# Kernel optimization log

Measured on AMD Instinct MI355X. Metric: run time of the kernel, lower is better.

## Reference

```python
import jax, jax.numpy as jnp
import numpy as np

SCOPE = 5
MASK_MAG = 9999.0


def setup_inputs() -> dict:
    key = jax.random.key(0)
    k1, k2, k3, k4 = jax.random.split(key, 4)
    B, T, F = 32, 2048, 256
    dataInput = jax.random.normal(k1, (B, T, F), dtype=jnp.float32)
    seqInput = jax.random.randint(k2, (B,), 1, T + 1)  # valid lengths in [1, T]
    seqInput = seqInput.at[0].set(T)  # torch code requires max(seqInput) == T
    W = jax.random.normal(k3, (SCOPE, F), dtype=jnp.float32) * 0.05  # Linear(F*scope -> 1) weight, reshaped
    b = jax.random.normal(k4, (1,), dtype=jnp.float32) * 0.05
    return {"dataInput": dataInput, "seqInput": seqInput, "W": W, "b": b,
            "hiddenNoduleNumbers": F}


def reference(dataInput, seqInput, W, b, hiddenNoduleNumbers):
    # dataInput: [B, T, F]; W: [scope, F]; b: [1]; seqInput: [B] lengths.
    B, T, F = dataInput.shape
    scope = W.shape[0]
    # Zero-pad `scope` frames at the end (torch pads scope rows then slices v:T+v).
    padded = jnp.concatenate(
        [dataInput, jnp.zeros((B, scope, F), dtype=dataInput.dtype)], axis=1)
    # Sliding-window linear score computed on-the-fly (no [B,T,scope*F] concat):
    # score[b,t] = sum_v padded[b, t+v, :] . W[v] + b
    scores = b[0] + sum(
        jnp.einsum('btf,f->bt', padded[:, v:T + v, :], W[v])
        for v in range(scope))  # [B, T]
    # AttentionMask: +9999 for valid positions, -9999 past the length; combined via min.
    valid = jnp.arange(T)[None, :] < seqInput[:, None]
    mask = jnp.where(valid, MASK_MAG, -MASK_MAG).astype(scores.dtype)
    maskedScores = jnp.minimum(scores, mask)
    attentionWeight = jax.nn.softmax(maskedScores, axis=-1)[:, :, None]  # [B, T, 1]
    attentionResult = jnp.sum(dataInput * attentionWeight, axis=1)  # [B, F]
    return attentionResult, attentionWeight
```

## Files before the change

kernel.cpp:

```cpp
#include <hip/hip_runtime.h>
#include <cfloat>

#define SCOPE 5
#define MASK_MAG 9999.0f
constexpr int F = 256;
constexpr int TW = 32;
constexpr int WAVES = 4;

__global__ __launch_bounds__(256) void fused_kernel(
    const float* __restrict__ data, const float* __restrict__ W,
    const float* __restrict__ bias, const int* __restrict__ seq,
    float* __restrict__ scores, float* __restrict__ pacc,
    float* __restrict__ pm, float* __restrict__ ps, int T) {
    const int b = blockIdx.y;
    const int tid = threadIdx.x;
    const int lane = tid & 63;
    const int wid = tid >> 6;
    const int lane4 = lane * 4;
    const int widx = blockIdx.x * WAVES + wid;
    const int t0 = widx * TW;
    if (t0 >= T) return;
    const int npw = T / TW;
    const float* __restrict__ dBase = data + (size_t)b * T * F;
    float* __restrict__ sb = scores + (size_t)b * T;
    const float bv = bias[0];
    const int L = seq[b];

    float4 w[SCOPE];
    #pragma unroll
    for (int v = 0; v < SCOPE; ++v)
        w[v] = *(const float4*)(W + v * F + lane4);

    const float4 fz = make_float4(0.f, 0.f, 0.f, 0.f);
    float4 S[16];

#define LOADROW(slot, off) do { \
    if ((off) < TW + 4) { \
        const int uu = t0 + (off); \
        S[slot] = (uu < T) ? *(const float4*)(dBase + (size_t)uu * F + lane4) : fz; \
    } } while (0)
#define DOT4(a, b) ((a).x*(b).x + (a).y*(b).y + (a).z*(b).z + (a).w*(b).w)

    #pragma unroll
    for (int k = 0; k < 16; ++k) LOADROW(k, k);

    float m_run = -FLT_MAX, s_run = 0.f;
    float4 acc = fz;

    #pragma unroll
    for (int ii = 0; ii < 2; ++ii) {
        const int base = ii * 16;
        float sc[8];

        #pragma unroll
        for (int j = 0; j < 8; ++j) {
            float s = DOT4(S[j], w[0]) + DOT4(S[j+1], w[1]) + DOT4(S[j+2], w[2])
                    + DOT4(S[j+3], w[3]) + DOT4(S[j+4], w[4]);
            s += __shfl_xor(s, 32, 64);
            s += __shfl_xor(s, 16, 64);
            s += __shfl_xor(s,  8, 64);
            s += __shfl_xor(s,  4, 64);
            s += __shfl_xor(s,  2, 64);
            s += __shfl_xor(s,  1, 64);
            s += bv;
            const int t = t0 + base + j;
            if (lane == 0) sb[t] = s;
            sc[j] = fminf(s, (t < L) ? MASK_MAG : -MASK_MAG);
        }
        {
            float gm = fmaxf(fmaxf(fmaxf(sc[0], sc[1]), fmaxf(sc[2], sc[3])),
                             fmaxf(fmaxf(sc[4], sc[5]), fmaxf(sc[6], sc[7])));
            const float m_new = fmaxf(m_run, gm);
            const float corr = expf(m_run - m_new);
            float psum = 0.f; float4 ga = fz;
            #pragma unroll
            for (int j = 0; j < 8; ++j) {
                const float p = expf(sc[j] - m_new);
                psum += p;
                ga.x += p * S[j].x; ga.y += p * S[j].y;
                ga.z += p * S[j].z; ga.w += p * S[j].w;
            }
            s_run = s_run * corr + psum;
            acc.x = acc.x * corr + ga.x; acc.y = acc.y * corr + ga.y;
            acc.z = acc.z * corr + ga.z; acc.w = acc.w * corr + ga.w;
            m_run = m_new;
        }
        #pragma unroll
        for (int k = 0; k < 8; ++k) LOADROW(k, base + 16 + k);

        #pragma unroll
        for (int j = 8; j < 16; ++j) {
            float s = DOT4(S[j & 15], w[0]) + DOT4(S[(j+1) & 15], w[1])
                    + DOT4(S[(j+2) & 15], w[2]) + DOT4(S[(j+3) & 15], w[3])
                    + DOT4(S[(j+4) & 15], w[4]);
            s += __shfl_xor(s, 32, 64);
            s += __shfl_xor(s, 16, 64);
            s += __shfl_xor(s,  8, 64);
            s += __shfl_xor(s,  4, 64);
            s += __shfl_xor(s,  2, 64);
            s += __shfl_xor(s,  1, 64);
            s += bv;
            const int t = t0 + base + j;
            if (lane == 0) sb[t] = s;
            sc[j - 8] = fminf(s, (t < L) ? MASK_MAG : -MASK_MAG);
        }
        {
            float gm = fmaxf(fmaxf(fmaxf(sc[0], sc[1]), fmaxf(sc[2], sc[3])),
                             fmaxf(fmaxf(sc[4], sc[5]), fmaxf(sc[6], sc[7])));
            const float m_new = fmaxf(m_run, gm);
            const float corr = expf(m_run - m_new);
            float psum = 0.f; float4 ga = fz;
            #pragma unroll
            for (int j = 0; j < 8; ++j) {
                const float p = expf(sc[j] - m_new);
                psum += p;
                ga.x += p * S[8 + j].x; ga.y += p * S[8 + j].y;
                ga.z += p * S[8 + j].z; ga.w += p * S[8 + j].w;
            }
            s_run = s_run * corr + psum;
            acc.x = acc.x * corr + ga.x; acc.y = acc.y * corr + ga.y;
            acc.z = acc.z * corr + ga.z; acc.w = acc.w * corr + ga.w;
            m_run = m_new;
        }
        #pragma unroll
        for (int k = 0; k < 8; ++k) LOADROW(8 + k, base + 24 + k);
    }
#undef DOT4
#undef LOADROW

    const int pw = b * npw + widx;
    *reinterpret_cast<float4*>(pacc + (size_t)pw * F + lane4) = acc;
    if (lane == 0) { pm[pw] = m_run; ps[pw] = s_run; }
}

__global__ __launch_bounds__(256) void finalize_kernel(
    const float* __restrict__ scores, const float* __restrict__ pacc,
    const float* __restrict__ pm, const float* __restrict__ ps,
    const int* __restrict__ seq, float* __restrict__ out_res,
    float* __restrict__ out_w, int T, int npw) {
    const int b = blockIdx.x;
    const int tid = threadIdx.x;
    __shared__ float scale[64];
    __shared__ float MS[2];

    if (tid < 64) {
        const float m = pm[b * npw + tid];
        const float s = ps[b * npw + tid];
        float M = m;
        #pragma unroll
        for (int off = 32; off >= 1; off >>= 1) M = fmaxf(M, __shfl_xor(M, off, 64));
        const float e = expf(m - M);
        float se = e * s;
        #pragma unroll
        for (int off = 32; off >= 1; off >>= 1) se += __shfl_xor(se, off, 64);
        scale[tid] = e;
        if (tid == 0) { MS[0] = M; MS[1] = 1.0f / se; }
    }
    __syncthreads();
    const float M = MS[0], invS = MS[1];

    float o = 0.f;
    for (int i = 0; i < npw; ++i)
        o += scale[i] * pacc[((size_t)(b * npw + i)) * F + tid];
    out_res[(size_t)b * F + tid] = o * invS;

    const int L = seq[b];
    for (int t = tid; t < T; t += 256) {
        const float raw = scores[(size_t)b * T + t];
        const float msk = fminf(raw, (t < L) ? MASK_MAG : -MASK_MAG);
        out_w[(size_t)b * T + t] = expf(msk - M) * invS;
    }
}

extern "C" void kernel_launch(void* const* d_in, const int* in_sizes, int n_in,
                              void* d_out, int out_size, void* d_ws, size_t ws_size,
                              hipStream_t stream) {
    const float* data = (const float*)d_in[0];
    const int*   seq  = (const int*)d_in[1];
    const float* W    = (const float*)d_in[2];
    const float* bias = (const float*)d_in[3];

    const int B  = in_sizes[1];
    const int Fr = in_sizes[2] / SCOPE;
    const int T  = in_sizes[0] / (B * Fr);
    (void)Fr;
    const int npw = T / TW;

    float* out_res = (float*)d_out;
    float* out_w   = (float*)d_out + (size_t)B * F;

    float* scores = (float*)d_ws;
    float* pacc   = scores + (size_t)B * T;
    float* pm     = pacc + (size_t)B * npw * F;
    float* ps     = pm + (size_t)B * npw;

    dim3 g1(T / (WAVES * TW), B);
    fused_kernel<<<g1, 256, 0, stream>>>(data, W, bias, seq, scores, pacc, pm, ps, T);
    finalize_kernel<<<B, 256, 0, stream>>>(scores, pacc, pm, ps, seq, out_res, out_w, T, npw);
}
```

Before: 35.37 us.

## Halve per-wave tile, merge partials in-block, split finalize across parts

```diff
diff --git a/kernel.cpp b/kernel.cpp
--- a/kernel.cpp
+++ b/kernel.cpp
@@ -4,10 +4,25 @@
 #define SCOPE 5
 #define MASK_MAG 9999.0f
 constexpr int F = 256;
-constexpr int TW = 32;
+constexpr int TW = 16;
 constexpr int WAVES = 4;
 
-__global__ __launch_bounds__(256) void fused_kernel(
+template <int CTRL>
+__device__ __forceinline__ float dppadd(float x) {
+    int v = __builtin_amdgcn_update_dpp(0, __float_as_int(x), CTRL, 0xF, 0xF, true);
+    return x + __int_as_float(v);
+}
+__device__ __forceinline__ float wave_sum(float s) {
+    s = dppadd<0xB1>(s);
+    s = dppadd<0x4E>(s);
+    s = dppadd<0x141>(s);
+    s = dppadd<0x140>(s);
+    s += __shfl_xor(s, 16, 64);
+    s += __shfl_xor(s, 32, 64);
+    return s;
+}
+
+__global__ __launch_bounds__(256, 4) void fused_kernel(
     const float* __restrict__ data, const float* __restrict__ W,
     const float* __restrict__ bias, const int* __restrict__ seq,
     float* __restrict__ scores, float* __restrict__ pacc,
@@ -17,10 +32,7 @@
     const int lane = tid & 63;
     const int wid = tid >> 6;
     const int lane4 = lane * 4;
-    const int widx = blockIdx.x * WAVES + wid;
-    const int t0 = widx * TW;
-    if (t0 >= T) return;
-    const int npw = T / TW;
+    const int t0 = (blockIdx.x * WAVES + wid) * TW;
     const float* __restrict__ dBase = data + (size_t)b * T * F;
     float* __restrict__ sb = scores + (size_t)b * T;
     const float bv = bias[0];
@@ -35,10 +47,9 @@
     float4 S[16];
 
 #define LOADROW(slot, off) do { \
-    if ((off) < TW + 4) { \
-        const int uu = t0 + (off); \
-        S[slot] = (uu < T) ? *(const float4*)(dBase + (size_t)uu * F + lane4) : fz; \
-    } } while (0)
+    const int uu = t0 + (off); \
+    S[slot] = (uu < T) ? *(const float4*)(dBase + (size_t)uu * F + lane4) : fz; \
+    } while (0)
 #define DOT4(a, b) ((a).x*(b).x + (a).y*(b).y + (a).z*(b).z + (a).w*(b).w)
 
     #pragma unroll
@@ -46,110 +57,107 @@
 
     float m_run = -FLT_MAX, s_run = 0.f;
     float4 acc = fz;
-
-    #pragma unroll
-    for (int ii = 0; ii < 2; ++ii) {
-        const int base = ii * 16;
-        float sc[8];
-
+    float sc[8];
+
+    #pragma unroll
+    for (int j = 0; j < 8; ++j) {
+        float s = DOT4(S[j], w[0]) + DOT4(S[j+1], w[1]) + DOT4(S[j+2], w[2])
+                + DOT4(S[j+3], w[3]) + DOT4(S[j+4], w[4]);
+        s = wave_sum(s) + bv;
+        const int t = t0 + j;
+        if (lane == 0) sb[t] = s;
+        sc[j] = fminf(s, (t < L) ? MASK_MAG : -MASK_MAG);
+    }
+    {
+        float gm = fmaxf(fmaxf(fmaxf(sc[0], sc[1]), fmaxf(sc[2], sc[3])),
+                         fmaxf(fmaxf(sc[4], sc[5]), fmaxf(sc[6], sc[7])));
+        const float m_new = fmaxf(m_run, gm);
+        const float corr = expf(m_run - m_new);
+        float psum = 0.f; float4 ga = fz;
         #pragma unroll
         for (int j = 0; j < 8; ++j) {
-            float s = DOT4(S[j], w[0]) + DOT4(S[j+1], w[1]) + DOT4(S[j+2], w[2])
-                    + DOT4(S[j+3], w[3]) + DOT4(S[j+4], w[4]);
-            s += __shfl_xor(s, 32, 64);
-            s += __shfl_xor(s, 16, 64);
-            s += __shfl_xor(s,  8, 64);
-            s += __shfl_xor(s,  4, 64);
-            s += __shfl_xor(s,  2, 64);
-            s += __shfl_xor(s,  1, 64);
-            s += bv;
-            const int t = t0 + base + j;
-            if (lane == 0) sb[t] = s;
-            sc[j] = fminf(s, (t < L) ? MASK_MAG : -MASK_MAG);
+            const float p = expf(sc[j] - m_new);
+            psum += p;
+            ga.x += p * S[j].x; ga.y += p * S[j].y;
+            ga.z += p * S[j].z; ga.w += p * S[j].w;
         }
-        {
-            float gm = fmaxf(fmaxf(fmaxf(sc[0], sc[1]), fmaxf(sc[2], sc[3])),
-                             fmaxf(fmaxf(sc[4], sc[5]), fmaxf(sc[6], sc[7])));
-            const float m_new = fmaxf(m_run, gm);
-            const float corr = expf(m_run - m_new);
-            float psum = 0.f; float4 ga = fz;
-            #pragma unroll
-            for (int j = 0; j < 8; ++j) {
-                const float p = expf(sc[j] - m_new);
-                psum += p;
-                ga.x += p * S[j].x; ga.y += p * S[j].y;
-                ga.z += p * S[j].z; ga.w += p * S[j].w;
-            }
-            s_run = s_run * corr + psum;
-            acc.x = acc.x * corr + ga.x; acc.y = acc.y * corr + ga.y;
-            acc.z = acc.z * corr + ga.z; acc.w = acc.w * corr + ga.w;
-            m_run = m_new;
+        s_run = s_run * corr + psum;
+        acc.x = acc.x * corr + ga.x; acc.y = acc.y * corr + ga.y;
+        acc.z = acc.z * corr + ga.z; acc.w = acc.w * corr + ga.w;
+        m_run = m_new;
+    }
+    #pragma unroll
+    for (int k = 0; k < 4; ++k) LOADROW(k, 16 + k);
+
+    #pragma unroll
+    for (int j = 0; j < 8; ++j) {
+        float s = DOT4(S[(8+j) & 15], w[0]) + DOT4(S[(9+j) & 15], w[1])
+                + DOT4(S[(10+j) & 15], w[2]) + DOT4(S[(11+j) & 15], w[3])
+                + DOT4(S[(12+j) & 15], w[4]);
+        s = wave_sum(s) + bv;
+        const int t = t0 + 8 + j;
+        if (lane == 0) sb[t] = s;
+        sc[j] = fminf(s, (t < L) ? MASK_MAG : -MASK_MAG);
+    }
+    {
+        float gm = fmaxf(fmaxf(fmaxf(sc[0], sc[1]), fmaxf(sc[2], sc[3])),
+                         fmaxf(fmaxf(sc[4], sc[5]), fmaxf(sc[6], sc[7])));
+        const float m_new = fmaxf(m_run, gm);
+        const float corr = expf(m_run - m_new);
+        float psum = 0.f; float4 ga = fz;
+        #pragma unroll
+        for (int j = 0; j < 8; ++j) {
+            const float p = expf(sc[j] - m_new);
+            psum += p;
+            ga.x += p * S[8 + j].x; ga.y += p * S[8 + j].y;
+            ga.z += p * S[8 + j].z; ga.w += p * S[8 + j].w;
         }
-        #pragma unroll
-        for (int k = 0; k < 8; ++k) LOADROW(k, base + 16 + k);
-
-        #pragma unroll
-        for (int j = 8; j < 16; ++j) {
-            float s = DOT4(S[j & 15], w[0]) + DOT4(S[(j+1) & 15], w[1])
-                    + DOT4(S[(j+2) & 15], w[2]) + DOT4(S[(j+3) & 15], w[3])
-                    + DOT4(S[(j+4) & 15], w[4]);
-            s += __shfl_xor(s, 32, 64);
-            s += __shfl_xor(s, 16, 64);
-            s += __shfl_xor(s,  8, 64);
-            s += __shfl_xor(s,  4, 64);
-            s += __shfl_xor(s,  2, 64);
-            s += __shfl_xor(s,  1, 64);
-            s += bv;
-            const int t = t0 + base + j;
-            if (lane == 0) sb[t] = s;
-            sc[j - 8] = fminf(s, (t < L) ? MASK_MAG : -MASK_MAG);
-        }
-        {
-            float gm = fmaxf(fmaxf(fmaxf(sc[0], sc[1]), fmaxf(sc[2], sc[3])),
-                             fmaxf(fmaxf(sc[4], sc[5]), fmaxf(sc[6], sc[7])));
-            const float m_new = fmaxf(m_run, gm);
-            const float corr = expf(m_run - m_new);
-            float psum = 0.f; float4 ga = fz;
-            #pragma unroll
-            for (int j = 0; j < 8; ++j) {
-                const float p = expf(sc[j] - m_new);
-                psum += p;
-                ga.x += p * S[8 + j].x; ga.y += p * S[8 + j].y;
-                ga.z += p * S[8 + j].z; ga.w += p * S[8 + j].w;
-            }
-            s_run = s_run * corr + psum;
-            acc.x = acc.x * corr + ga.x; acc.y = acc.y * corr + ga.y;
-            acc.z = acc.z * corr + ga.z; acc.w = acc.w * corr + ga.w;
-            m_run = m_new;
-        }
-        #pragma unroll
-        for (int k = 0; k < 8; ++k) LOADROW(8 + k, base + 24 + k);
+        s_run = s_run * corr + psum;
+        acc.x = acc.x * corr + ga.x; acc.y = acc.y * corr + ga.y;
+        acc.z = acc.z * corr + ga.z; acc.w = acc.w * corr + ga.w;
+        m_run = m_new;
     }
 #undef DOT4
 #undef LOADROW
 
-    const int pw = b * npw + widx;
-    *reinterpret_cast<float4*>(pacc + (size_t)pw * F + lane4) = acc;
-    if (lane == 0) { pm[pw] = m_run; ps[pw] = s_run; }
+    __shared__ float macc[WAVES][F];
+    __shared__ float mm[WAVES], ss[WAVES];
+    *reinterpret_cast<float4*>(&macc[wid][lane4]) = acc;
+    if (lane == 0) { mm[wid] = m_run; ss[wid] = s_run; }
+    __syncthreads();
+
+    const float M = fmaxf(fmaxf(mm[0], mm[1]), fmaxf(mm[2], mm[3]));
+    float e0 = expf(mm[0] - M), e1 = expf(mm[1] - M);
+    float e2 = expf(mm[2] - M), e3 = expf(mm[3] - M);
+    const float s_blk = e0 * ss[0] + e1 * ss[1] + e2 * ss[2] + e3 * ss[3];
+
+    const int blk = blockIdx.x;
+    const int npb = gridDim.x;
+    const float ab = e0 * macc[0][tid] + e1 * macc[1][tid]
+                   + e2 * macc[2][tid] + e3 * macc[3][tid];
+    pacc[((size_t)(b * npb + blk)) * F + tid] = ab;
+    if (tid == 0) { pm[b * npb + blk] = M; ps[b * npb + blk] = s_blk; }
 }
 
 __global__ __launch_bounds__(256) void finalize_kernel(
     const float* __restrict__ scores, const float* __restrict__ pacc,
     const float* __restrict__ pm, const float* __restrict__ ps,
     const int* __restrict__ seq, float* __restrict__ out_res,
-    float* __restrict__ out_w, int T, int npw) {
+    float* __restrict__ out_w, int T, int npb) {
     const int b = blockIdx.x;
+    const int part = blockIdx.y;
     const int tid = threadIdx.x;
+    __shared__ float MS[2];
     __shared__ float scale[64];
-    __shared__ float MS[2];
 
     if (tid < 64) {
-        const float m = pm[b * npw + tid];
-        const float s = ps[b * npw + tid];
+        const bool v = tid < npb;
+        const float m = v ? pm[b * npb + tid] : -FLT_MAX;
+        const float s = v ? ps[b * npb + tid] : 0.f;
         float M = m;
         #pragma unroll
         for (int off = 32; off >= 1; off >>= 1) M = fmaxf(M, __shfl_xor(M, off, 64));
-        const float e = expf(m - M);
+        const float e = v ? expf(m - M) : 0.f;
         float se = e * s;
         #pragma unroll
         for (int off = 32; off >= 1; off >>= 1) se += __shfl_xor(se, off, 64);
@@ -159,16 +167,20 @@
     __syncthreads();
     const float M = MS[0], invS = MS[1];
 
-    float o = 0.f;
-    for (int i = 0; i < npw; ++i)
-        o += scale[i] * pacc[((size_t)(b * npw + i)) * F + tid];
-    out_res[(size_t)b * F + tid] = o * invS;
-
-    const int L = seq[b];
-    for (int t = tid; t < T; t += 256) {
-        const float raw = scores[(size_t)b * T + t];
-        const float msk = fminf(raw, (t < L) ? MASK_MAG : -MASK_MAG);
-        out_w[(size_t)b * T + t] = expf(msk - M) * invS;
+    if (part == 0) {
+        float o = 0.f;
+        for (int i = 0; i < npb; ++i)
+            o += scale[i] * pacc[((size_t)(b * npb + i)) * F + tid];
+        out_res[(size_t)b * F + tid] = o * invS;
+    } else {
+        const int L = seq[b];
+        const int chunk = T / 8;
+        const int tbase = (part - 1) * chunk;
+        for (int t = tbase + tid; t < tbase + chunk; t += 256) {
+            const float raw = scores[(size_t)b * T + t];
+            const float msk = fminf(raw, (t < L) ? MASK_MAG : -MASK_MAG);
+            out_w[(size_t)b * T + t] = expf(msk - M) * invS;
+        }
     }
 }
 
@@ -184,17 +196,18 @@
     const int Fr = in_sizes[2] / SCOPE;
     const int T  = in_sizes[0] / (B * Fr);
     (void)Fr;
-    const int npw = T / TW;
+    const int npb = T / (WAVES * TW);
 
     float* out_res = (float*)d_out;
     float* out_w   = (float*)d_out + (size_t)B * F;
 
     float* scores = (float*)d_ws;
     float* pacc   = scores + (size_t)B * T;
-    float* pm     = pacc + (size_t)B * npw * F;
-    float* ps     = pm + (size_t)B * npw;
-
-    dim3 g1(T / (WAVES * TW), B);
+    float* pm     = pacc + (size_t)B * npb * F;
+    float* ps     = pm + (size_t)B * npb;
+
+    dim3 g1(npb, B);
     fused_kernel<<<g1, 256, 0, stream>>>(data, W, bias, seq, scores, pacc, pm, ps, T);
-    finalize_kernel<<<B, 256, 0, stream>>>(scores, pacc, pm, ps, seq, out_res, out_w, T, npw);
-}
+    dim3 g2(B, 9);
+    finalize_kernel<<<g2, 256, 0, stream>>>(scores, pacc, pm, ps, seq, out_res, out_w, T, npb);
+}
```

Measured after the change: 38.03 us. 1.08x slower.
